# Kernel optimization log

Measured on AMD Instinct MI355X. Metric: run time of the kernel, lower is better.

Reference implementation:

```python
import jax, jax.numpy as jnp
import numpy as np

TOP_K = 3
EPS = 1e-12  # F.normalize eps


def _lstm(x, W_ih, W_hh, b_ih, b_hh):
    # x: [B, S, I]; PyTorch gate order i, f, g, o; returns h sequence [B, S, H]
    B = x.shape[0]
    H = W_hh.shape[1]
    xs = jnp.swapaxes(x, 0, 1)  # [S, B, I]
    x_proj = xs @ W_ih.T + b_ih + b_hh  # [S, B, 4H]

    def step(carry, xp):
        h, c = carry
        gates = xp + h @ W_hh.T
        i, f, g, o = jnp.split(gates, 4, axis=-1)
        i = jax.nn.sigmoid(i); f = jax.nn.sigmoid(f)
        g = jnp.tanh(g); o = jax.nn.sigmoid(o)
        c = f * c + i * g
        h = o * jnp.tanh(c)
        return (h, c), h

    init = (jnp.zeros((B, H), x.dtype), jnp.zeros((B, H), x.dtype))
    _, hs = jax.lax.scan(step, init, x_proj)
    return jnp.swapaxes(hs, 0, 1)  # [B, S, H]


def setup_inputs() -> dict:
    key = jax.random.key(0)
    ks = jax.random.split(key, 16)
    B, S, I, H, M, N, O = 4, 256, 512, 1024, 256, 65536, 512
    sc = 0.02
    return {
        "x": jax.random.normal(ks[0], (B, S, I), jnp.float32),
        "keys": jax.random.normal(ks[1], (N, M), jnp.float32),
        "values": jax.random.normal(ks[2], (N, M), jnp.float32),
        "importance": jnp.ones((N,), jnp.float32),
        "W_ih": jax.random.normal(ks[3], (4 * H, I), jnp.float32) * sc,
        "W_hh": jax.random.normal(ks[4], (4 * H, H), jnp.float32) * sc,
        "b_ih": jnp.zeros((4 * H,), jnp.float32),
        "b_hh": jnp.zeros((4 * H,), jnp.float32),
        "Wq": jax.random.normal(ks[5], (M, H), jnp.float32) * sc,
        "bq": jnp.zeros((M,), jnp.float32),
        "Wa": jax.random.normal(ks[6], (1, M), jnp.float32) * sc,
        "ba": jnp.zeros((1,), jnp.float32),
        "Wc": jax.random.normal(ks[7], (M, M), jnp.float32) * sc,
        "bc": jnp.zeros((M,), jnp.float32),
        "Wo": jax.random.normal(ks[8], (O, H + M), jnp.float32) * sc,
        "bo": jnp.zeros((O,), jnp.float32),
    }


def reference(x, keys, values, importance, W_ih, W_hh, b_ih, b_hh,
              Wq, bq, Wa, ba, Wc, bc, Wo, bo):
    # Controller LSTM over the whole sequence
    h = _lstm(x, W_ih, W_hh, b_ih, b_hh)  # [B, S, H]

    # Query projection and cosine similarity against the memory keys
    q = h @ Wq.T + bq  # [B, S, M]
    qn = q / jnp.maximum(jnp.linalg.norm(q, axis=-1, keepdims=True), EPS)
    kn = keys / jnp.maximum(jnp.linalg.norm(keys, axis=-1, keepdims=True), EPS)
    sim = jnp.einsum("bsm,nm->bsn", qn, kn) * importance  # [B, S, N]

    # Top-k retrieval and value gather
    _, top_idx = jax.lax.top_k(sim, TOP_K)  # [B, S, k]
    retrieved = values[top_idx]  # [B, S, k, M]

    # Learned attention over retrieved memories
    att_logits = (retrieved @ Wa.T + ba)[..., 0]  # [B, S, k]
    att = jax.nn.softmax(att_logits, axis=-1)
    mem = jnp.einsum("bsk,bskm->bsm", att, retrieved)
    mem = mem @ Wc.T + bc  # combine_layer

    out = jnp.concatenate([h, mem], axis=-1) @ Wo.T + bo  # [B, S, O]
    return out
```

## Files before the change

### kernel.cpp

```cpp
#include <hip/hip_runtime.h>
#include <hip/hip_bf16.h>
#include <cstdint>
#include <cstddef>

#define BB 4
#define SS 256
#define ID 512
#define HD 1024
#define MD 256
#define NKEY 65536
#define OD 512
#define ROWS 1024
#define NWG_LSTM 256
#define NTH_LSTM 256
#define KPB 2048
#define KSPLITS (NKEY / KPB)

typedef __attribute__((ext_vector_type(8))) short bf16x8;
typedef __attribute__((ext_vector_type(4))) float f32x4;
typedef __attribute__((ext_vector_type(8))) unsigned short u16x8;

__global__ __launch_bounds__(256) void sgemm_nt(
    const float* __restrict__ A, int lda,
    const float* __restrict__ Bm, int ldb,
    float* __restrict__ C, int ldc, int K,
    const float* __restrict__ bias, const float* __restrict__ bias2,
    int accum)
{
    __shared__ float As[64][17];
    __shared__ float Bs[64][17];
    const int t = threadIdx.x;
    const int tx = t & 15, ty = t >> 4;
    const int bm = blockIdx.y << 6, bn = blockIdx.x << 6;
    const int lrow = t >> 2, lk4 = (t & 3) << 2;
    float acc[4][4] = {};

    for (int kb = 0; kb < K; kb += 16) {
        const float4 av = *(const float4*)&A[(size_t)(bm + lrow) * lda + kb + lk4];
        const float4 bv = *(const float4*)&Bm[(size_t)(bn + lrow) * ldb + kb + lk4];
        __syncthreads();
        As[lrow][lk4 + 0] = av.x; As[lrow][lk4 + 1] = av.y;
        As[lrow][lk4 + 2] = av.z; As[lrow][lk4 + 3] = av.w;
        Bs[lrow][lk4 + 0] = bv.x; Bs[lrow][lk4 + 1] = bv.y;
        Bs[lrow][lk4 + 2] = bv.z; Bs[lrow][lk4 + 3] = bv.w;
        __syncthreads();
#pragma unroll
        for (int k = 0; k < 16; ++k) {
            const float a0 = As[4 * ty + 0][k], a1 = As[4 * ty + 1][k];
            const float a2 = As[4 * ty + 2][k], a3 = As[4 * ty + 3][k];
            const float b0 = Bs[4 * tx + 0][k], b1 = Bs[4 * tx + 1][k];
            const float b2 = Bs[4 * tx + 2][k], b3 = Bs[4 * tx + 3][k];
            acc[0][0] += a0 * b0; acc[0][1] += a0 * b1; acc[0][2] += a0 * b2; acc[0][3] += a0 * b3;
            acc[1][0] += a1 * b0; acc[1][1] += a1 * b1; acc[1][2] += a1 * b2; acc[1][3] += a1 * b3;
            acc[2][0] += a2 * b0; acc[2][1] += a2 * b1; acc[2][2] += a2 * b2; acc[2][3] += a2 * b3;
            acc[3][0] += a3 * b0; acc[3][1] += a3 * b1; acc[3][2] += a3 * b2; acc[3][3] += a3 * b3;
        }
    }

#pragma unroll
    for (int i = 0; i < 4; ++i) {
        const int row = bm + 4 * ty + i;
        const int col = bn + 4 * tx;
        float4* cp = (float4*)&C[(size_t)row * ldc + col];
        float4 r;
        if (accum) {
            const float4 old = *cp;
            r.x = old.x + acc[i][0]; r.y = old.y + acc[i][1];
            r.z = old.z + acc[i][2]; r.w = old.w + acc[i][3];
        } else {
            float bx = bias[col + 0], by = bias[col + 1], bz = bias[col + 2], bw = bias[col + 3];
            if (bias2) { bx += bias2[col + 0]; by += bias2[col + 1]; bz += bias2[col + 2]; bw += bias2[col + 3]; }
            r.x = acc[i][0] + bx; r.y = acc[i][1] + by;
            r.z = acc[i][2] + bz; r.w = acc[i][3] + bw;
        }
        *cp = r;
    }
}

__global__ __launch_bounds__(256) void sgemm_nt_w(
    const float* __restrict__ A, const float* __restrict__ Bm,
    float* __restrict__ C, const float* __restrict__ bias, const float* __restrict__ bias2)
{
    __shared__ float As[16][64];
    __shared__ float Bs[16][128];
    const int t = threadIdx.x;
    const int tx = t & 15, ty = t >> 4;
    const int bm = blockIdx.y << 6, bn = blockIdx.x << 7;
    const int arow = t & 63, akq = t >> 6;
    const int brow = t & 127, bkq = t >> 7;
    float acc[4][8] = {};

    for (int kb = 0; kb < 512; kb += 16) {
        const float4 av  = *(const float4*)&A[(size_t)(bm + arow) * 512 + kb + (akq << 2)];
        const float4 bv0 = *(const float4*)&Bm[(size_t)(bn + brow) * 512 + kb + (bkq << 3)];
        const float4 bv1 = *(const float4*)&Bm[(size_t)(bn + brow) * 512 + kb + (bkq << 3) + 4];
        __syncthreads();
        As[(akq << 2) + 0][arow] = av.x; As[(akq << 2) + 1][arow] = av.y;
        As[(akq << 2) + 2][arow] = av.z; As[(akq << 2) + 3][arow] = av.w;
        Bs[(bkq << 3) + 0][brow] = bv0.x; Bs[(bkq << 3) + 1][brow] = bv0.y;
        Bs[(bkq << 3) + 2][brow] = bv0.z; Bs[(bkq << 3) + 3][brow] = bv0.w;
        Bs[(bkq << 3) + 4][brow] = bv1.x; Bs[(bkq << 3) + 5][brow] = bv1.y;
        Bs[(bkq << 3) + 6][brow] = bv1.z; Bs[(bkq << 3) + 7][brow] = bv1.w;
        __syncthreads();
#pragma unroll
        for (int k = 0; k < 16; ++k) {
            const float4 a  = *(const float4*)&As[k][ty << 2];
            const float4 b0 = *(const float4*)&Bs[k][tx << 3];
            const float4 b1 = *(const float4*)&Bs[k][(tx << 3) + 4];
            acc[0][0] += a.x * b0.x; acc[0][1] += a.x * b0.y; acc[0][2] += a.x * b0.z; acc[0][3] += a.x * b0.w;
            acc[0][4] += a.x * b1.x; acc[0][5] += a.x * b1.y; acc[0][6] += a.x * b1.z; acc[0][7] += a.x * b1.w;
            acc[1][0] += a.y * b0.x; acc[1][1] += a.y * b0.y; acc[1][2] += a.y * b0.z; acc[1][3] += a.y * b0.w;
            acc[1][4] += a.y * b1.x; acc[1][5] += a.y * b1.y; acc[1][6] += a.y * b1.z; acc[1][7] += a.y * b1.w;
            acc[2][0] += a.z * b0.x; acc[2][1] += a.z * b0.y; acc[2][2] += a.z * b0.z; acc[2][3] += a.z * b0.w;
            acc[2][4] += a.z * b1.x; acc[2][5] += a.z * b1.y; acc[2][6] += a.z * b1.z; acc[2][7] += a.z * b1.w;
            acc[3][0] += a.w * b0.x; acc[3][1] += a.w * b0.y; acc[3][2] += a.w * b0.z; acc[3][3] += a.w * b0.w;
            acc[3][4] += a.w * b1.x; acc[3][5] += a.w * b1.y; acc[3][6] += a.w * b1.z; acc[3][7] += a.w * b1.w;
        }
    }

#pragma unroll
    for (int i = 0; i < 4; ++i) {
        const int row = bm + (ty << 2) + i;
        const int col = bn + (tx << 3);
        float4 r0, r1;
        r0.x = acc[i][0] + bias[col + 0] + bias2[col + 0];
        r0.y = acc[i][1] + bias[col + 1] + bias2[col + 1];
        r0.z = acc[i][2] + bias[col + 2] + bias2[col + 2];
        r0.w = acc[i][3] + bias[col + 3] + bias2[col + 3];
        r1.x = acc[i][4] + bias[col + 4] + bias2[col + 4];
        r1.y = acc[i][5] + bias[col + 5] + bias2[col + 5];
        r1.z = acc[i][6] + bias[col + 6] + bias2[col + 6];
        r1.w = acc[i][7] + bias[col + 7] + bias2[col + 7];
        *(float4*)&C[(size_t)row * 4096 + col] = r0;
        *(float4*)&C[(size_t)row * 4096 + col + 4] = r1;
    }
}

__device__ inline unsigned pack_bf16(float a, float b) {
    return (__float_as_uint(a) >> 16) | (__float_as_uint(b) & 0xFFFF0000u);
}

__global__ void rownorm(const float* __restrict__ X, const float* __restrict__ imp,
                        float* __restrict__ scale_out, float* __restrict__ Xn,
                        unsigned short* __restrict__ kb, int nrows)
{
    const int row = blockIdx.x * 4 + (threadIdx.x >> 6);
    const int lane = threadIdx.x & 63;
    if (row >= nrows) return;
    float4 v = *(const float4*)&X[(size_t)row * 256 + (lane << 2)];
    float ss = v.x * v.x + v.y * v.y + v.z * v.z + v.w * v.w;
#pragma unroll
    for (int o = 1; o < 64; o <<= 1) ss += __shfl_xor(ss, o);
    float sc = 1.f / fmaxf(sqrtf(ss), 1e-12f);
    if (imp) sc *= imp[row];
    if (scale_out && lane == 0) scale_out[row] = sc;
    if (Xn) {
        v.x *= sc; v.y *= sc; v.z *= sc; v.w *= sc;
        *(float4*)&Xn[(size_t)row * 256 + (lane << 2)] = v;
    }
    if (kb) {
        uint2 p;
        p.x = pack_bf16(v.x * sc, v.y * sc);
        p.y = pack_bf16(v.z * sc, v.w * sc);
        *(uint2*)&kb[(size_t)row * 256 + (lane << 2)] = p;
    }
}

__device__ inline float sigm_f(float x) { return 1.f / (1.f + __expf(-x)); }
__device__ inline float tanh_f(float x) { return 1.f - 2.f / (__expf(2.f * x) + 1.f); }

#define SUBSTEP(B, U, UN, C4, XPC) do {                                           \
    asm volatile("s_waitcnt vmcnt(3)" ::: "memory");                              \
    __builtin_amdgcn_sched_barrier(0);                                            \
    const unsigned* pb_ = rec + (slot << 12) + (B << 10) + (t << 2);              \
    while ((((U.x ^ st) | (U.y ^ st) | (U.z ^ st) | (U.w ^ st)) & 0xFFu) != 0u) { \
        __builtin_amdgcn_s_sleep(1);                                              \
        asm volatile("global_load_dwordx4 %0, %1, off sc0 sc1\n\ts_waitcnt vmcnt(0)" \
                     : "=&v"(U) : "v"(pb_) : "memory");                           \
    }                                                                             \
    {                                                                             \
        float4 hw_;                                                               \
        hw_.x = __uint_as_float(U.x & 0xFFFFFF00u);                               \
        hw_.y = __uint_as_float(U.y & 0xFFFFFF00u);                               \
        hw_.z = __uint_as_float(U.z & 0xFFFFFF00u);                               \
        hw_.w = __uint_as_float(U.w & 0xFFFFFF00u);                               \
        *(float4*)&h_lds[B][t << 2] = hw_;                                        \
    }                                                                             \
    asm volatile("s_waitcnt lgkmcnt(0)" ::: "memory");                            \
    __builtin_amdgcn_sched_barrier(0);                                            \
    __builtin_amdgcn_s_barrier();                                                 \
    {                                                                             \
        const unsigned* pn_ = rec + (((B == 3) ? (slot ^ 1) : slot) << 12)        \
                              + (((B + 1) & 3) << 10) + (t << 2);                 \
        asm volatile("global_load_dwordx4 %0, %1, off sc0 sc1"                    \
                     : "=&v"(UN) : "v"(pn_) : "memory");                          \
    }                                                                             \
    const float* hb_ = &h_lds[B][0];                                              \
    float ax_ = 0.f, ay_ = 0.f, az_ = 0.f, aw_ = 0.f;                             \
    _Pragma("unroll")                                                             \
    for (int j = 0; j < 16; ++j) {                                                \
        const float4 hv_ = *(const float4*)&hb_[(ksub << 2) + (j << 6)];          \
        ax_ += w4[j].x * hv_.x; ay_ += w4[j].y * hv_.y;                           \
        az_ += w4[j].z * hv_.z; aw_ += w4[j].w * hv_.w;                           \
    }                                                                             \
    float sm_ = (ax_ + ay_) + (az_ + aw_);                                        \
    sm_ += __shfl_xor(sm_, 1); sm_ += __shfl_xor(sm_, 2);                         \
    sm_ += __shfl_xor(sm_, 4); sm_ += __shfl_xor(sm_, 8);                         \
    sm_ += XPC;                                                                   \
    const float vi_ = __shfl(sm_, ksub);                                          \
    const float vf_ = __shfl(sm_, ksub + 16);                                     \
    const float vg_ = __shfl(sm_, ksub + 32);                                     \
    const float vo_ = __shfl(sm_, ksub + 48);                                     \
    const float iv_ = sigm_f(vi_), fv_ = sigm_f(vf_);                             \
    const float gv_ = tanh_f(vg_), ov_ = sigm_f(vo_);                             \
    C4 = fv_ * C4 + iv_ * gv_;                                                    \
    const float hvv_ = ov_ * tanh_f(C4);                                          \
    if (lane == 0) {                                                              \
        unsigned* dst_ = rec + ((slot ^ 1) << 12) + (B << 10) + unit;             \
        const unsigned uv_ = (__float_as_uint(hvv_) & 0xFFFFFF00u) |              \
                             ((unsigned)(s + 1) & 0xFFu);                         \
        float* ha_ = &h_all[(size_t)((B << 8) + s) * 1024 + unit];                \
        asm volatile("global_store_dword %0, %1, off sc0 sc1"                     \
                     :: "v"(dst_), "v"(uv_) : "memory");                          \
        asm volatile("global_store_dword %0, %1, off"                             \
                     :: "v"(ha_), "v"(hvv_) : "memory");                          \
    }                                                                             \
    {                                                                             \
        const float* px_ = &xp[(size_t)((B << 8) + sn) * 4096 + wrow];            \
        asm volatile("global_load_dword %0, %1, off"                              \
                     : "=&v"(XPC) : "v"(px_) : "memory");                         \
    }                                                                             \
} while (0)

__global__ __launch_bounds__(256) void lstm_kernel(
    const float* __restrict__ xp, const float* __restrict__ W_hh,
    unsigned* __restrict__ rec, float* __restrict__ h_all)
{
    __shared__ float h_lds[4][1024];
    const int t = threadIdx.x;
    const int wave = t >> 6, lane = t & 63;
    const int gt = lane >> 4, ksub = lane & 15;
    const int unit = (blockIdx.x << 2) + wave;
    const int wrow = (gt << 10) + unit;

    float4 w4[16];
#pragma unroll
    for (int j = 0; j < 16; ++j)
        w4[j] = *(const float4*)&W_hh[(size_t)wrow * 1024 + (ksub << 2) + (j << 6)];

    float c40 = 0.f, c41 = 0.f, c42 = 0.f, c43 = 0.f;
    float xpc0 = xp[(size_t)(0 * 256 + 0) * 4096 + wrow];
    float xpc1 = xp[(size_t)(1 * 256 + 0) * 4096 + wrow];
    float xpc2 = xp[(size_t)(2 * 256 + 0) * 4096 + wrow];
    float xpc3 = xp[(size_t)(3 * 256 + 0) * 4096 + wrow];

    uint4 u0 = make_uint4(~0u, ~0u, ~0u, ~0u);
    uint4 u1 = u0, u2 = u0, u3 = u0;

    {
        const unsigned* p00 = rec + (t << 2);
        asm volatile("global_load_dwordx4 %0, %1, off sc0 sc1\n\ts_waitcnt vmcnt(0)"
                     : "=&v"(u0) : "v"(p00) : "memory");
        __builtin_amdgcn_sched_barrier(0);
    }

    for (int s = 0; s < 256; ++s) {
        const int slot = s & 1;
        const unsigned st = (unsigned)s & 0xFFu;
        const int sn = (s < 255) ? s + 1 : 255;
        SUBSTEP(0, u0, u1, c40, xpc0);
        SUBSTEP(1, u1, u2, c41, xpc1);
        SUBSTEP(2, u2, u3, c42, xpc2);
        SUBSTEP(3, u3, u0, c43, xpc3);
    }
}

#define SWAP1(A, B, IA, IB) { float _t = A; A = B; B = _t; int _u = IA; IA = IB; IB = _u; }
#define INS8G(P, V, ID) do {                                          \
    const float _v = (V); const int _id = (ID);                       \
    if (_v > P##v7) {                                                 \
        P##v7 = _v; P##i7 = _id;                                      \
        if (P##v7 > P##v6) SWAP1(P##v6, P##v7, P##i6, P##i7);         \
        if (P##v6 > P##v5) SWAP1(P##v5, P##v6, P##i5, P##i6);         \
        if (P##v5 > P##v4) SWAP1(P##v4, P##v5, P##i4, P##i5);         \
        if (P##v4 > P##v3) SWAP1(P##v3, P##v4, P##i3, P##i4);         \
        if (P##v3 > P##v2) SWAP1(P##v2, P##v3, P##i2, P##i3);         \
        if (P##v2 > P##v1) SWAP1(P##v1, P##v2, P##i1, P##i2);         \
        if (P##v1 > P##v0) SWAP1(P##v0, P##v1, P##i0, P##i1);         \
    }                                                                 \
} while (0)
#define DECL8(P) float P##v0=-3e38f,P##v1=-3e38f,P##v2=-3e38f,P##v3=-3e38f, \
                       P##v4=-3e38f,P##v5=-3e38f,P##v6=-3e38f,P##v7=-3e38f; \
                 int P##i0=0x7fffffff,P##i1=0x7fffffff,P##i2=0x7fffffff,P##i3=0x7fffffff, \
                     P##i4=0x7fffffff,P##i5=0x7fffffff,P##i6=0x7fffffff,P##i7=0x7fffffff;

__global__ __launch_bounds__(256) void sim_mfma_b(
    const float* __restrict__ qn, const unsigned short* __restrict__ kb,
    float* __restrict__ part_v8, int* __restrict__ part_i8)
{
    __shared__ unsigned short k_lds[64 * 264];
    __shared__ float cand_v[256 * 8];
    __shared__ int   cand_i[256 * 8];
    const int t = threadIdx.x;
    const int wave = t >> 6, lane = t & 63;
    const int ks = blockIdx.x, qs = blockIdx.y;
    const int key_base = ks * KPB;
    const int q0 = qs << 6;
    const int qrow = q0 + (wave << 4) + (lane & 15);
    const int kg = lane >> 4;

    bf16x8 bq[8];
#pragma unroll
    for (int kc = 0; kc < 8; ++kc) {
        const float* qp = &qn[(size_t)qrow * 256 + (kc << 5) + (kg << 3)];
        const float4 f0 = *(const float4*)qp;
        const float4 f1 = *(const float4*)(qp + 4);
        union { unsigned int u[4]; bf16x8 h; } cv;
        cv.u[0] = pack_bf16(f0.x, f0.y);
        cv.u[1] = pack_bf16(f0.z, f0.w);
        cv.u[2] = pack_bf16(f1.x, f1.y);
        cv.u[3] = pack_bf16(f1.z, f1.w);
        bq[kc] = cv.h;
    }

    DECL8(t)

    const int srow = t >> 2, scol0 = (t & 3) << 6;

    for (int stg = 0; stg < KPB / 64; ++stg) {
        __syncthreads();
        {
            const unsigned short* kp = &kb[(size_t)(key_base + (stg << 6) + srow) * 256 + scol0];
#pragma unroll
            for (int i = 0; i < 8; ++i)
                *(u16x8*)&k_lds[srow * 264 + scol0 + (i << 3)] = *(const u16x8*)(kp + (i << 3));
        }
        __syncthreads();

#pragma unroll
        for (int kt = 0; kt < 4; ++kt) {
            f32x4 a0 = {0.f, 0.f, 0.f, 0.f};
            f32x4 a1 = {0.f, 0.f, 0.f, 0.f};
#pragma unroll
            for (int kc = 0; kc < 4; ++kc) {
                const bf16x8 af = *(const bf16x8*)&k_lds[((kt << 4) + (lane & 15)) * 264 +
                                                         (kc << 5) + (kg << 3)];
                a0 = __builtin_amdgcn_mfma_f32_16x16x32_bf16(af, bq[kc], a0, 0, 0, 0);
            }
#pragma unroll
            for (int kc = 4; kc < 8; ++kc) {
                const bf16x8 af = *(const bf16x8*)&k_lds[((kt << 4) + (lane & 15)) * 264 +
                                                         (kc << 5) + (kg << 3)];
                a1 = __builtin_amdgcn_mfma_f32_16x16x32_bf16(af, bq[kc], a1, 0, 0, 0);
            }
            const int kidx = key_base + (stg << 6) + (kt << 4) + (kg << 2);
            INS8G(t, a0[0] + a1[0], kidx + 0);
            INS8G(t, a0[1] + a1[1], kidx + 1);
            INS8G(t, a0[2] + a1[2], kidx + 2);
            INS8G(t, a0[3] + a1[3], kidx + 3);
        }
    }

    __syncthreads();
    cand_v[t * 8 + 0] = tv0; cand_i[t * 8 + 0] = ti0;
    cand_v[t * 8 + 1] = tv1; cand_i[t * 8 + 1] = ti1;
    cand_v[t * 8 + 2] = tv2; cand_i[t * 8 + 2] = ti2;
    cand_v[t * 8 + 3] = tv3; cand_i[t * 8 + 3] = ti3;
    cand_v[t * 8 + 4] = tv4; cand_i[t * 8 + 4] = ti4;
    cand_v[t * 8 + 5] = tv5; cand_i[t * 8 + 5] = ti5;
    cand_v[t * 8 + 6] = tv6; cand_i[t * 8 + 6] = ti6;
    cand_v[t * 8 + 7] = tv7; cand_i[t * 8 + 7] = ti7;
    __syncthreads();
    if (t < 64) {
        DECL8(m)
        const int w = t >> 4, c = t & 15;
        for (int g = 0; g < 4; ++g) {
            const int src = ((w << 6) + c + (g << 4)) * 8;
            for (int r = 0; r < 8; ++r)
                INS8G(m, cand_v[src + r], cand_i[src + r]);
        }
        const size_t base = (size_t)(q0 + t) * (KSPLITS * 8) + ks * 8;
        part_v8[base + 0] = mv0; part_i8[base + 0] = mi0;
        part_v8[base + 1] = mv1; part_i8[base + 1] = mi1;
        part_v8[base + 2] = mv2; part_i8[base + 2] = mi2;
        part_v8[base + 3] = mv3; part_i8[base + 3] = mi3;
        part_v8[base + 4] = mv4; part_i8[base + 4] = mi4;
        part_v8[base + 5] = mv5; part_i8[base + 5] = mi5;
        part_v8[base + 6] = mv6; part_i8[base + 6] = mi6;
        part_v8[base + 7] = mv7; part_i8[base + 7] = mi7;
    }
}

__global__ __launch_bounds__(256) void sim_mfma_f(
    const float* __restrict__ qn, const float* __restrict__ keys,
    const float* __restrict__ rnk, float* __restrict__ part_v8, int* __restrict__ part_i8)
{
    __shared__ unsigned short k_lds[64 * 264];
    __shared__ float cand_v[256 * 8];
    __shared__ int   cand_i[256 * 8];
    const int t = threadIdx.x;
    const int wave = t >> 6, lane = t & 63;
    const int ks = blockIdx.x, qs = blockIdx.y;
    const int key_base = ks * KPB;
    const int q0 = qs << 6;
    const int qrow = q0 + (wave << 4) + (lane & 15);
    const int kg = lane >> 4;

    bf16x8 bq[8];
#pragma unroll
    for (int kc = 0; kc < 8; ++kc) {
        const float* qp = &qn[(size_t)qrow * 256 + (kc << 5) + (kg << 3)];
        const float4 f0 = *(const float4*)qp;
        const float4 f1 = *(const float4*)(qp + 4);
        union { unsigned int u[4]; bf16x8 h; } cv;
        cv.u[0] = pack_bf16(f0.x, f0.y);
        cv.u[1] = pack_bf16(f0.z, f0.w);
        cv.u[2] = pack_bf16(f1.x, f1.y);
        cv.u[3] = pack_bf16(f1.z, f1.w);
        bq[kc] = cv.h;
    }

    DECL8(t)

    for (int stg = 0; stg < KPB / 64; ++stg) {
        __syncthreads();
#pragma unroll
        for (int i = 0; i < 8; ++i) {
            const int g = (i << 11) + (t << 3);
            const int row = g >> 8, col = g & 255;
            const int krow = key_base + (stg << 6) + row;
            const float sc = rnk[krow];
            const float* kp = &keys[(size_t)krow * 256 + col];
            float4 f0 = *(const float4*)kp;
            float4 f1 = *(const float4*)(kp + 4);
            f0.x *= sc; f0.y *= sc; f0.z *= sc; f0.w *= sc;
            f1.x *= sc; f1.y *= sc; f1.z *= sc; f1.w *= sc;
            union { unsigned int u[4]; u16x8 h; } cv;
            cv.u[0] = pack_bf16(f0.x, f0.y);
            cv.u[1] = pack_bf16(f0.z, f0.w);
            cv.u[2] = pack_bf16(f1.x, f1.y);
            cv.u[3] = pack_bf16(f1.z, f1.w);
            *(u16x8*)&k_lds[row * 264 + col] = cv.h;
        }
        __syncthreads();

#pragma unroll
        for (int kt = 0; kt < 4; ++kt) {
            f32x4 a0 = {0.f, 0.f, 0.f, 0.f};
            f32x4 a1 = {0.f, 0.f, 0.f, 0.f};
#pragma unroll
            for (int kc = 0; kc < 4; ++kc) {
                const bf16x8 af = *(const bf16x8*)&k_lds[((kt << 4) + (lane & 15)) * 264 +
                                                         (kc << 5) + (kg << 3)];
                a0 = __builtin_amdgcn_mfma_f32_16x16x32_bf16(af, bq[kc], a0, 0, 0, 0);
            }
#pragma unroll
            for (int kc = 4; kc < 8; ++kc) {
                const bf16x8 af = *(const bf16x8*)&k_lds[((kt << 4) + (lane & 15)) * 264 +
                                                         (kc << 5) + (kg << 3)];
                a1 = __builtin_amdgcn_mfma_f32_16x16x32_bf16(af, bq[kc], a1, 0, 0, 0);
            }
            const int kidx = key_base + (stg << 6) + (kt << 4) + (kg << 2);
            INS8G(t, a0[0] + a1[0], kidx + 0);
            INS8G(t, a0[1] + a1[1], kidx + 1);
            INS8G(t, a0[2] + a1[2], kidx + 2);
            INS8G(t, a0[3] + a1[3], kidx + 3);
        }
    }

    __syncthreads();
    cand_v[t * 8 + 0] = tv0; cand_i[t * 8 + 0] = ti0;
    cand_v[t * 8 + 1] = tv1; cand_i[t * 8 + 1] = ti1;
    cand_v[t * 8 + 2] = tv2; cand_i[t * 8 + 2] = ti2;
    cand_v[t * 8 + 3] = tv3; cand_i[t * 8 + 3] = ti3;
    cand_v[t * 8 + 4] = tv4; cand_i[t * 8 + 4] = ti4;
    cand_v[t * 8 + 5] = tv5; cand_i[t * 8 + 5] = ti5;
    cand_v[t * 8 + 6] = tv6; cand_i[t * 8 + 6] = ti6;
    cand_v[t * 8 + 7] = tv7; cand_i[t * 8 + 7] = ti7;
    __syncthreads();
    if (t < 64) {
        DECL8(m)
        const int w = t >> 4, c = t & 15;
        for (int g = 0; g < 4; ++g) {
            const int src = ((w << 6) + c + (g << 4)) * 8;
            for (int r = 0; r < 8; ++r)
                INS8G(m, cand_v[src + r], cand_i[src + r]);
        }
        const size_t base = (size_t)(q0 + t) * (KSPLITS * 8) + ks * 8;
        part_v8[base + 0] = mv0; part_i8[base + 0] = mi0;
        part_v8[base + 1] = mv1; part_i8[base + 1] = mi1;
        part_v8[base + 2] = mv2; part_i8[base + 2] = mi2;
        part_v8[base + 3] = mv3; part_i8[base + 3] = mi3;
        part_v8[base + 4] = mv4; part_i8[base + 4] = mi4;
        part_v8[base + 5] = mv5; part_i8[base + 5] = mi5;
        part_v8[base + 6] = mv6; part_i8[base + 6] = mi6;
        part_v8[base + 7] = mv7; part_i8[base + 7] = mi7;
    }
}

__global__ void cand_merge(const float* __restrict__ part_v8, const int* __restrict__ part_i8,
                           int* __restrict__ cand8_i)
{
    const int q = blockIdx.x * 256 + threadIdx.x;
    if (q >= ROWS) return;
    DECL8(c)
    for (int j = 0; j < KSPLITS * 8; ++j)
        INS8G(c, part_v8[(size_t)q * (KSPLITS * 8) + j], part_i8[(size_t)q * (KSPLITS * 8) + j]);
    cand8_i[q * 8 + 0] = ci0; cand8_i[q * 8 + 1] = ci1;
    cand8_i[q * 8 + 2] = ci2; cand8_i[q * 8 + 3] = ci3;
    cand8_i[q * 8 + 4] = ci4; cand8_i[q * 8 + 5] = ci5;
    cand8_i[q * 8 + 6] = ci6; cand8_i[q * 8 + 7] = ci7;
}

__global__ void rescore_gather(const float* __restrict__ qn, const float* __restrict__ keys,
                               const float* __restrict__ rnk, const int* __restrict__ cand8_i,
                               const float* __restrict__ values, const float* __restrict__ Wa,
                               const float* __restrict__ ba, float* __restrict__ mem_raw)
{
    const int q = blockIdx.x;
    const int lane = threadIdx.x;
    const float4 qv = *(const float4*)&qn[(size_t)q * 256 + (lane << 2)];
    float s0, s1, s2, s3, s4, s5, s6, s7;
    int j0, j1, j2, j3, j4, j5, j6, j7;
#define RES(R, S, J) { J = cand8_i[q * 8 + R]; \
    const float4 kv = *(const float4*)&keys[(size_t)J * 256 + (lane << 2)]; \
    float d = qv.x * kv.x + qv.y * kv.y + qv.z * kv.z + qv.w * kv.w; \
    d += __shfl_xor(d, 1); d += __shfl_xor(d, 2); d += __shfl_xor(d, 4); \
    d += __shfl_xor(d, 8); d += __shfl_xor(d, 16); d += __shfl_xor(d, 32); \
    S = d * rnk[J]; }
    RES(0, s0, j0) RES(1, s1, j1) RES(2, s2, j2) RES(3, s3, j3)
    RES(4, s4, j4) RES(5, s5, j5) RES(6, s6, j6) RES(7, s7, j7)
#undef RES
    int top[3];
#define BET(SV, JV) if (SV > bv || (SV == bv && JV < bi)) { bv = SV; bi = JV; }
#pragma unroll
    for (int k = 0; k < 3; ++k) {
        float bv = s0; int bi = j0;
        BET(s1, j1) BET(s2, j2) BET(s3, j3) BET(s4, j4)
        BET(s5, j5) BET(s6, j6) BET(s7, j7)
        top[k] = bi;
        if (j0 == bi) s0 = -3e38f;
        if (j1 == bi) s1 = -3e38f;
        if (j2 == bi) s2 = -3e38f;
        if (j3 == bi) s3 = -3e38f;
        if (j4 == bi) s4 = -3e38f;
        if (j5 == bi) s5 = -3e38f;
        if (j6 == bi) s6 = -3e38f;
        if (j7 == bi) s7 = -3e38f;
    }
#undef BET
    const float4 wa = *(const float4*)&Wa[lane << 2];
    float4 vr[3];
    float lg[3];
#pragma unroll
    for (int r = 0; r < 3; ++r) {
        const float4 v = *(const float4*)&values[(size_t)top[r] * 256 + (lane << 2)];
        vr[r] = v;
        float d = v.x * wa.x + v.y * wa.y + v.z * wa.z + v.w * wa.w;
#pragma unroll
        for (int o = 1; o < 64; o <<= 1) d += __shfl_xor(d, o);
        lg[r] = d + ba[0];
    }
    const float mx = fmaxf(lg[0], fmaxf(lg[1], lg[2]));
    float e0 = __expf(lg[0] - mx), e1 = __expf(lg[1] - mx), e2 = __expf(lg[2] - mx);
    const float inv = 1.f / (e0 + e1 + e2);
    e0 *= inv; e1 *= inv; e2 *= inv;
    float4 m;
    m.x = e0 * vr[0].x + e1 * vr[1].x + e2 * vr[2].x;
    m.y = e0 * vr[0].y + e1 * vr[1].y + e2 * vr[2].y;
    m.z = e0 * vr[0].z + e1 * vr[1].z + e2 * vr[2].z;
    m.w = e0 * vr[0].w + e1 * vr[1].w + e2 * vr[2].w;
    *(float4*)&mem_raw[(size_t)q * 256 + (lane << 2)] = m;
}

extern "C" void kernel_launch(void* const* d_in, const int* in_sizes, int n_in,
                              void* d_out, int out_size, void* d_ws, size_t ws_size,
                              hipStream_t stream)
{
    (void)in_sizes; (void)n_in; (void)out_size;
    const float* x     = (const float*)d_in[0];
    const float* keys  = (const float*)d_in[1];
    const float* values= (const float*)d_in[2];
    const float* imp   = (const float*)d_in[3];
    const float* W_ih  = (const float*)d_in[4];
    const float* W_hh  = (const float*)d_in[5];
    const float* b_ih  = (const float*)d_in[6];
    const float* b_hh  = (const float*)d_in[7];
    const float* Wq    = (const float*)d_in[8];
    const float* bq    = (const float*)d_in[9];
    const float* Wa    = (const float*)d_in[10];
    const float* ba    = (const float*)d_in[11];
    const float* Wc    = (const float*)d_in[12];
    const float* bc    = (const float*)d_in[13];
    const float* Wo    = (const float*)d_in[14];
    const float* bo    = (const float*)d_in[15];
    float* out = (float*)d_out;

    float* ws = (float*)d_ws;
    size_t o = 0;
    float* xp      = ws + o; o += (size_t)1024 * 4096;
    float* h_all   = ws + o; o += (size_t)1024 * 1024;
    unsigned* rec  = (unsigned*)(ws + o); o += 2 * 4096;
    float* rnk     = ws + o; o += NKEY;
    float* qbuf    = ws + o; o += (size_t)ROWS * 256;
    float* qn      = ws + o; o += (size_t)ROWS * 256;
    float* part_v8 = ws + o; o += (size_t)ROWS * KSPLITS * 8;
    int*   part_i8 = (int*)(ws + o); o += (size_t)ROWS * KSPLITS * 8;
    int*   cand8_i = (int*)(ws + o); o += ROWS * 8;
    float* mem_raw = ws + o; o += (size_t)ROWS * 256;
    float* memb    = ws + o; o += (size_t)ROWS * 256;
    unsigned short* kb = (unsigned short*)(ws + o);
    const size_t need_bf16 = (o + (size_t)NKEY * 256 / 2) * sizeof(float);
    const bool use_bf16 = ws_size >= need_bf16;

    hipMemsetAsync(rec, 0, 2 * 4096 * 4, stream);

    rownorm<<<NKEY / 4, 256, 0, stream>>>(keys, imp, rnk, nullptr,
                                          use_bf16 ? kb : nullptr, NKEY);

    sgemm_nt_w<<<dim3(32, 16), 256, 0, stream>>>(x, W_ih, xp, b_ih, b_hh);

    lstm_kernel<<<NWG_LSTM, NTH_LSTM, 0, stream>>>(xp, W_hh, rec, h_all);

    sgemm_nt<<<dim3(4, 16), 256, 0, stream>>>(h_all, HD, Wq, HD, qbuf, MD, HD, bq, nullptr, 0);

    rownorm<<<ROWS / 4, 256, 0, stream>>>(qbuf, nullptr, nullptr, qn, nullptr, ROWS);

    if (use_bf16)
        sim_mfma_b<<<dim3(KSPLITS, 16), 256, 0, stream>>>(qn, kb, part_v8, part_i8);
    else
        sim_mfma_f<<<dim3(KSPLITS, 16), 256, 0, stream>>>(qn, keys, rnk, part_v8, part_i8);
    cand_merge<<<ROWS / 256, 256, 0, stream>>>(part_v8, part_i8, cand8_i);
    rescore_gather<<<ROWS, 64, 0, stream>>>(qn, keys, rnk, cand8_i, values, Wa, ba, mem_raw);

    sgemm_nt<<<dim3(4, 16), 256, 0, stream>>>(mem_raw, MD, Wc, MD, memb, MD, MD, bc, nullptr, 0);

    sgemm_nt<<<dim3(8, 16), 256, 0, stream>>>(h_all, HD, Wo, HD + MD, out, OD, HD, bo, nullptr, 0);
    sgemm_nt<<<dim3(8, 16), 256, 0, stream>>>(memb, MD, Wo + HD, HD + MD, out, OD, MD, nullptr, nullptr, 1);
}
```

Measured before the change: 1.344 ms.

## Overlap key normalization with the persistent LSTM via extra workgroups

The key-normalization and bf16 packing pass moves from a separate kernel launch into extra workgroups appended to the LSTM launch. Those blocks normalize 256 key rows each, so the work can run on otherwise idle CUs while the latency-bound recurrent LSTM spins on its cross-workgroup sync. The risk is that the extra blocks compete for CUs, or get scheduled before some LSTM blocks, and delay the LSTM's spin-wait handshakes. The rownorm kernel is reduced to the query-only path.

```diff
diff --git a/kernel.cpp b/kernel.cpp
--- a/kernel.cpp
+++ b/kernel.cpp
@@ -140,9 +140,7 @@
     return (__float_as_uint(a) >> 16) | (__float_as_uint(b) & 0xFFFF0000u);
 }
 
-__global__ void rownorm(const float* __restrict__ X, const float* __restrict__ imp,
-                        float* __restrict__ scale_out, float* __restrict__ Xn,
-                        unsigned short* __restrict__ kb, int nrows)
+__global__ void rownorm(const float* __restrict__ X, float* __restrict__ Xn, int nrows)
 {
     const int row = blockIdx.x * 4 + (threadIdx.x >> 6);
     const int lane = threadIdx.x & 63;
@@ -151,19 +149,9 @@
     float ss = v.x * v.x + v.y * v.y + v.z * v.z + v.w * v.w;
 #pragma unroll
     for (int o = 1; o < 64; o <<= 1) ss += __shfl_xor(ss, o);
-    float sc = 1.f / fmaxf(sqrtf(ss), 1e-12f);
-    if (imp) sc *= imp[row];
-    if (scale_out && lane == 0) scale_out[row] = sc;
-    if (Xn) {
-        v.x *= sc; v.y *= sc; v.z *= sc; v.w *= sc;
-        *(float4*)&Xn[(size_t)row * 256 + (lane << 2)] = v;
-    }
-    if (kb) {
-        uint2 p;
-        p.x = pack_bf16(v.x * sc, v.y * sc);
-        p.y = pack_bf16(v.z * sc, v.w * sc);
-        *(uint2*)&kb[(size_t)row * 256 + (lane << 2)] = p;
-    }
+    const float sc = 1.f / fmaxf(sqrtf(ss), 1e-12f);
+    v.x *= sc; v.y *= sc; v.z *= sc; v.w *= sc;
+    *(float4*)&Xn[(size_t)row * 256 + (lane << 2)] = v;
 }
 
 __device__ inline float sigm_f(float x) { return 1.f / (1.f + __expf(-x)); }
@@ -234,10 +222,34 @@
 
 __global__ __launch_bounds__(256) void lstm_kernel(
     const float* __restrict__ xp, const float* __restrict__ W_hh,
-    unsigned* __restrict__ rec, float* __restrict__ h_all)
+    unsigned* __restrict__ rec, float* __restrict__ h_all,
+    const float* __restrict__ keys, const float* __restrict__ imp,
+    float* __restrict__ rnk, unsigned short* __restrict__ kb)
 {
     __shared__ float h_lds[4][1024];
     const int t = threadIdx.x;
+
+    if (blockIdx.x >= NWG_LSTM) {
+        const int base_row = (blockIdx.x - NWG_LSTM) << 8;
+        const int lane = t & 63;
+        for (int it = 0; it < 64; ++it) {
+            const int row = base_row + (it << 2) + (t >> 6);
+            float4 v = *(const float4*)&keys[(size_t)row * 256 + (lane << 2)];
+            float ss = v.x * v.x + v.y * v.y + v.z * v.z + v.w * v.w;
+#pragma unroll
+            for (int o = 1; o < 64; o <<= 1) ss += __shfl_xor(ss, o);
+            const float sc = imp[row] / fmaxf(sqrtf(ss), 1e-12f);
+            if (lane == 0) rnk[row] = sc;
+            if (kb) {
+                uint2 p;
+                p.x = pack_bf16(v.x * sc, v.y * sc);
+                p.y = pack_bf16(v.z * sc, v.w * sc);
+                *(uint2*)&kb[(size_t)row * 256 + (lane << 2)] = p;
+            }
+        }
+        return;
+    }
+
     const int wave = t >> 6, lane = t & 63;
     const int gt = lane >> 4, ksub = lane & 15;
     const int unit = (blockIdx.x << 2) + wave;
@@ -615,16 +627,14 @@
 
     hipMemsetAsync(rec, 0, 2 * 4096 * 4, stream);
 
-    rownorm<<<NKEY / 4, 256, 0, stream>>>(keys, imp, rnk, nullptr,
-                                          use_bf16 ? kb : nullptr, NKEY);
-
     sgemm_nt_w<<<dim3(32, 16), 256, 0, stream>>>(x, W_ih, xp, b_ih, b_hh);
 
-    lstm_kernel<<<NWG_LSTM, NTH_LSTM, 0, stream>>>(xp, W_hh, rec, h_all);
+    lstm_kernel<<<2 * NWG_LSTM, NTH_LSTM, 0, stream>>>(
+        xp, W_hh, rec, h_all, keys, imp, rnk, use_bf16 ? kb : nullptr);
 
     sgemm_nt<<<dim3(4, 16), 256, 0, stream>>>(h_all, HD, Wq, HD, qbuf, MD, HD, bq, nullptr, 0);
 
-    rownorm<<<ROWS / 4, 256, 0, stream>>>(qbuf, nullptr, nullptr, qn, nullptr, ROWS);
+    rownorm<<<ROWS / 4, 256, 0, stream>>>(qbuf, qn, ROWS);
 
     if (use_bf16)
         sim_mfma_b<<<dim3(KSPLITS, 16), 256, 0, stream>>>(qn, kb, part_v8, part_i8);
```

Result: no change. 1.325 ms (-1.4%).
